# Kernel tuning notes

Hardware: AMD Instinct MI355X
Metric: run time of the kernel (lower is better)

Reference implementation:

```python
import jax, jax.numpy as jnp
import numpy as np
import math

D_MODEL = 1024
NHEAD = 16
D_K = D_MODEL // NHEAD
B, S = 4, 2048


def _stable_softmax(scores):
    # faithful to the source: max-subtract, exp, divide by (sum + 1e-10)
    m = jnp.max(scores, axis=-1, keepdims=True)
    e = jnp.exp(scores - m)
    return e / (jnp.sum(e, axis=-1, keepdims=True) + 1e-10)


def setup_inputs() -> dict:
    key = jax.random.key(0)
    ks = jax.random.split(key, 11)
    gain = math.sqrt(2.0)
    # xavier_uniform: bound = gain * sqrt(6/(fan_in+fan_out)) = gain*sqrt(6/(2*d))
    bound = gain * math.sqrt(6.0 / (2 * D_MODEL))
    def xavier(k):
        return jax.random.uniform(k, (D_MODEL, D_MODEL), jnp.float32, -bound, bound)
    return {
        "q": jax.random.normal(ks[0], (B, S, D_MODEL), jnp.float32),
        "k": jax.random.normal(ks[1], (B, S, D_MODEL), jnp.float32),
        "v": jax.random.normal(ks[2], (B, S, D_MODEL), jnp.float32),
        "Wq": xavier(ks[3]), "bq": jnp.zeros((D_MODEL,), jnp.float32),
        "Wk": xavier(ks[4]), "bk": jnp.zeros((D_MODEL,), jnp.float32),
        "Wv": xavier(ks[5]), "bv": jnp.zeros((D_MODEL,), jnp.float32),
        "Wo": xavier(ks[6]), "bo": jnp.zeros((D_MODEL,), jnp.float32),
    }


def reference(q, k, v, Wq, bq, Wk, bk, Wv, bv, Wo, bo):
    b = q.shape[0]
    # linear projections (torch Linear: x @ W.T + b)
    Q = q @ Wq.T + bq
    K = k @ Wk.T + bk
    V = v @ Wv.T + bv
    # [B, H, S, d_k]
    Q = Q.reshape(b, -1, NHEAD, D_K).transpose(0, 2, 1, 3)
    K = K.reshape(b, -1, NHEAD, D_K).transpose(0, 2, 1, 3)
    V = V.reshape(b, -1, NHEAD, D_K).transpose(0, 2, 1, 3)
    scores = jnp.einsum("bhqd,bhkd->bhqk", Q / math.sqrt(D_K), K)
    attn_weight = _stable_softmax(scores)  # dropout p=0 -> identity
    attn = jnp.einsum("bhqk,bhkd->bhqd", attn_weight, V)
    concat = attn.transpose(0, 2, 1, 3).reshape(b, -1, D_MODEL)
    return concat @ Wo.T + bo
```

## Files before the change

kernel.cpp:

```cpp
#include <hip/hip_runtime.h>

#define DMODEL 1024
#define NH 16
#define DK 64
#define NB 4
#define SEQ 2048
#define MTOT (NB*SEQ)

typedef __attribute__((ext_vector_type(8))) short bf16x8;
typedef __attribute__((ext_vector_type(4))) short s16x4;
typedef __attribute__((ext_vector_type(4))) float f32x4;
typedef __attribute__((ext_vector_type(4))) float f4;
typedef __attribute__((ext_vector_type(4))) unsigned short us4;
typedef __attribute__((ext_vector_type(8))) unsigned short us8;
typedef __attribute__((ext_vector_type(2))) unsigned int u32x2;
typedef const __attribute__((address_space(1))) void* as1cv;
typedef __attribute__((address_space(3))) void* as3v;

__device__ __forceinline__ unsigned short f2bf(float f){
  union { float f; unsigned u; } v; v.f = f;
  unsigned r = v.u + 0x7FFFu + ((v.u >> 16) & 1u);
  return (unsigned short)(r >> 16);
}

__device__ __forceinline__ unsigned cvt_pk_bf16(float lo, float hi){
  unsigned r;
  asm("v_cvt_pk_bf16_f32 %0, %1, %2" : "=v"(r) : "v"(lo), "v"(hi));
  return r;
}

__device__ __forceinline__ f32x4 mfma16(s16x4 a, s16x4 b, f32x4 c){
#if __has_builtin(__builtin_amdgcn_mfma_f32_16x16x16bf16_1k)
  return __builtin_amdgcn_mfma_f32_16x16x16bf16_1k(a, b, c, 0, 0, 0);
#else
  asm("v_mfma_f32_16x16x16_bf16 %0, %1, %2, %0" : "+v"(c) : "v"(a), "v"(b));
  return c;
#endif
}

__global__ __launch_bounds__(256) void cvt_kernel(const float* __restrict__ src,
                                                  unsigned short* __restrict__ dst, int n4){
  int i = blockIdx.x*256 + threadIdx.x;
  if (i >= n4) return;
  f4 f = ((const f4*)src)[i];
  us4 o;
  o.x = f2bf(f.x); o.y = f2bf(f.y); o.z = f2bf(f.z); o.w = f2bf(f.w);
  ((us4*)dst)[i] = o;
}

template<int MODE, int AF32>
__global__ __launch_bounds__(256) void gemm_bt(const void* __restrict__ Aptr,
    const unsigned short* __restrict__ Bw, const float* __restrict__ bias,
    void* __restrict__ dst, float scale)
{
  __shared__ __align__(16) unsigned short sA[128*32];
  __shared__ __align__(16) unsigned short sB[128*32];
  const int tid = threadIdx.x;
  const int lane = tid & 63;
  const int w = tid >> 6;
  const int m0 = blockIdx.y * 128;
  const int n0 = blockIdx.x * 128;
  const int fr = lane & 15;
  const int kg = lane >> 4;
  const int msub = (w & 1) * 64;
  const int nsub = (w >> 1) * 64;

  f32x4 acc[4][4];
#pragma unroll
  for (int i = 0; i < 4; i++)
#pragma unroll
    for (int j = 0; j < 4; j++) acc[i][j] = f32x4{0.f,0.f,0.f,0.f};

  for (int kt = 0; kt < DMODEL; kt += 32){
#pragma unroll
    for (int j = 0; j < 2; j++){
      const int idx = j*256 + tid;
      const int row = idx >> 2;
      const int cg  = (idx & 3) << 3;
      if (AF32){
        const float* ap = (const float*)Aptr + (size_t)(m0+row)*DMODEL + kt + cg;
        f4 f0 = *(const f4*)ap;
        f4 f1 = *(const f4*)(ap + 4);
        us8 o;
        o[0]=f2bf(f0.x); o[1]=f2bf(f0.y); o[2]=f2bf(f0.z); o[3]=f2bf(f0.w);
        o[4]=f2bf(f1.x); o[5]=f2bf(f1.y); o[6]=f2bf(f1.z); o[7]=f2bf(f1.w);
        *((us8*)sA + idx) = o;
      } else {
        const unsigned short* ap = (const unsigned short*)Aptr + (size_t)(m0+row)*DMODEL + kt + cg;
        __builtin_amdgcn_global_load_lds((as1cv)ap, (as3v)(&sA[(size_t)idx*8]), 16, 0, 0);
      }
      const unsigned short* bp = Bw + (size_t)(n0+row)*DMODEL + kt + cg;
      __builtin_amdgcn_global_load_lds((as1cv)bp, (as3v)(&sB[(size_t)idx*8]), 16, 0, 0);
    }
    __syncthreads();
    bf16x8 af[4], bfr[4];
#pragma unroll
    for (int f = 0; f < 4; f++)
      af[f] = *(const bf16x8*)&sA[(msub + f*16 + fr)*32 + kg*8];
#pragma unroll
    for (int f = 0; f < 4; f++)
      bfr[f] = *(const bf16x8*)&sB[(nsub + f*16 + fr)*32 + kg*8];
#pragma unroll
    for (int i = 0; i < 4; i++)
#pragma unroll
      for (int j = 0; j < 4; j++)
        acc[i][j] = __builtin_amdgcn_mfma_f32_16x16x32_bf16(af[i], bfr[j], acc[i][j], 0, 0, 0);
    __syncthreads();
  }

#pragma unroll
  for (int i = 0; i < 4; i++){
#pragma unroll
    for (int j = 0; j < 4; j++){
      const int n = n0 + nsub + j*16 + fr;
      const float bv = bias[n];
      if (MODE == 1){
        const int m = m0 + msub + i*16 + kg*4;
        const int b = m >> 11, s = m & (SEQ-1);
        const int h = n >> 6,  d = n & (DK-1);
        us4 pk;
#pragma unroll
        for (int r = 0; r < 4; r++) pk[r] = f2bf(acc[i][j][r] + bv);
        *(us4*)&((unsigned short*)dst)[((size_t)(b*NH+h)*DK + d)*SEQ + s] = pk;
      } else {
#pragma unroll
        for (int r = 0; r < 4; r++){
          const int m = m0 + msub + i*16 + kg*4 + r;
          float vacc = acc[i][j][r] + bv;
          if (MODE == 2){
            ((float*)dst)[(size_t)m*DMODEL + n] = vacc;
          } else {
            const int b = m >> 11, s = m & (SEQ-1);
            const int h = n >> 6,  d = n & (DK-1);
            ((unsigned short*)dst)[((size_t)(b*NH + h)*SEQ + s)*DK + d] = f2bf(vacc * scale);
          }
        }
      }
    }
  }
}

__global__ __launch_bounds__(256) void attn_kernel(const unsigned short* __restrict__ Qh,
    const unsigned short* __restrict__ Kh, const unsigned short* __restrict__ VTh,
    unsigned short* __restrict__ attnO)
{
  const int tid = threadIdx.x;
  const int lane = tid & 63;
  const int w = tid >> 6;
  const int fr = lane & 15;
  const int kg = lane >> 4;
  const int bid = blockIdx.x;
  const int swz = (bid & 7) * 128 + (bid >> 3);
  const int bh = swz >> 4;
  const int qt = (swz & 15) * 128 + w * 32;

  const unsigned short* Qb = Qh + ((size_t)bh*SEQ + qt)*DK;
  const unsigned short* Kb = Kh + (size_t)bh*SEQ*DK + (size_t)fr*DK + kg*8;
  const unsigned short* Vb = VTh + (size_t)bh*DK*SEQ + kg*4;

  bf16x8 qf[2][2];
#pragma unroll
  for (int qh = 0; qh < 2; qh++){
    qf[qh][0] = *(const bf16x8*)(Qb + (qh*16 + fr)*DK + kg*8);
    qf[qh][1] = *(const bf16x8*)(Qb + (qh*16 + fr)*DK + 32 + kg*8);
  }

  f32x4 o[2][4];
#pragma unroll
  for (int qh = 0; qh < 2; qh++)
#pragma unroll
    for (int nd = 0; nd < 4; nd++) o[qh][nd] = f32x4{0.f,0.f,0.f,0.f};
  float mr[2] = {-1e30f, -1e30f};
  float lr[2] = {0.f, 0.f};

  for (int kt = 0; kt < SEQ; kt += 64){
    f32x4 s[2][4];
#pragma unroll
    for (int n = 0; n < 4; n++){
      const unsigned short* kp = Kb + (size_t)(kt + n*16)*DK;
      bf16x8 k0 = *(const bf16x8*)kp;
      bf16x8 k1 = *(const bf16x8*)(kp + 32);
#pragma unroll
      for (int qh = 0; qh < 2; qh++){
        f32x4 z = f32x4{0.f,0.f,0.f,0.f};
        z         = __builtin_amdgcn_mfma_f32_16x16x32_bf16(k0, qf[qh][0], z, 0, 0, 0);
        s[qh][n]  = __builtin_amdgcn_mfma_f32_16x16x32_bf16(k1, qf[qh][1], s[qh][n] = z, 0, 0, 0);
      }
    }

    unsigned pk[2][4][2];
#pragma unroll
    for (int qh = 0; qh < 2; qh++){
      float tm = -1e30f;
#pragma unroll
      for (int n = 0; n < 4; n++)
#pragma unroll
        for (int r = 0; r < 4; r++) tm = fmaxf(tm, s[qh][n][r]);
      tm = fmaxf(tm, __shfl_xor(tm, 16));
      tm = fmaxf(tm, __shfl_xor(tm, 32));
      const bool defer = __all(tm - mr[qh] <= 8.0f);
      float aal = 1.0f;
      if (!defer){
        const float mn = fmaxf(mr[qh], tm);
        aal = exp2f(mr[qh] - mn);
        mr[qh] = mn;
      }
      float p[4][4];
      float rs = 0.f;
#pragma unroll
      for (int n = 0; n < 4; n++)
#pragma unroll
        for (int r = 0; r < 4; r++){
          p[n][r] = exp2f(s[qh][n][r] - mr[qh]);
          rs += p[n][r];
        }
      rs += __shfl_xor(rs, 16);
      rs += __shfl_xor(rs, 32);
      lr[qh] = lr[qh]*aal + rs;
      if (!defer){
        f32x4 alv;
#pragma unroll
        for (int r = 0; r < 4; r++) alv[r] = __shfl(aal, kg*4 + r, 64);
#pragma unroll
        for (int nd = 0; nd < 4; nd++) o[qh][nd] *= alv;
      }
#pragma unroll
      for (int n = 0; n < 4; n++){
        pk[qh][n][0] = cvt_pk_bf16(p[n][0], p[n][1]);
        pk[qh][n][1] = cvt_pk_bf16(p[n][2], p[n][3]);
      }
    }

#pragma unroll
    for (int nd = 0; nd < 4; nd++){
      const unsigned short* vp = Vb + (size_t)(nd*16 + fr)*SEQ + kt;
      s16x4 vf[4];
#pragma unroll
      for (int ks = 0; ks < 4; ks++) vf[ks] = *(const s16x4*)(vp + ks*16);
#pragma unroll
      for (int ks = 0; ks < 4; ks++){
#pragma unroll
        for (int qh = 0; qh < 2; qh++){
          union { u32x2 u; s16x4 s; } pa;
          pa.u = u32x2{pk[qh][ks][0], pk[qh][ks][1]};
          o[qh][nd] = mfma16(pa.s, vf[ks], o[qh][nd]);
        }
      }
    }
  }

  const int b = bh >> 4, h = bh & (NH-1);
#pragma unroll
  for (int qh = 0; qh < 2; qh++){
    const float invl = 1.f / (lr[qh] + 1e-10f);
    f32x4 iv;
#pragma unroll
    for (int r = 0; r < 4; r++) iv[r] = __shfl(invl, kg*4 + r, 64);
#pragma unroll
    for (int r = 0; r < 4; r++){
      const int srow = qt + qh*16 + kg*4 + r;
      const size_t base = ((size_t)b*SEQ + srow)*DMODEL + (size_t)h*DK;
#pragma unroll
      for (int nd = 0; nd < 4; nd++)
        attnO[base + nd*16 + fr] = f2bf(o[qh][nd][r] * iv[r]);
    }
  }
}

extern "C" void kernel_launch(void* const* d_in, const int* in_sizes, int n_in,
                              void* d_out, int out_size, void* d_ws, size_t ws_size,
                              hipStream_t stream)
{
  const float* q  = (const float*)d_in[0];
  const float* k  = (const float*)d_in[1];
  const float* v  = (const float*)d_in[2];
  const float* Wq = (const float*)d_in[3];
  const float* bq = (const float*)d_in[4];
  const float* Wk = (const float*)d_in[5];
  const float* bk = (const float*)d_in[6];
  const float* Wv = (const float*)d_in[7];
  const float* bv = (const float*)d_in[8];
  const float* Wo = (const float*)d_in[9];
  const float* bo = (const float*)d_in[10];

  char* ws = (char*)d_ws;
  const size_t WSZ = (size_t)DMODEL*DMODEL*2;
  const size_t SZ  = (size_t)MTOT*DMODEL*2;
  unsigned short* wqb   = (unsigned short*)(ws);
  unsigned short* wkb   = (unsigned short*)(ws + WSZ);
  unsigned short* wvb   = (unsigned short*)(ws + 2*WSZ);
  unsigned short* wob   = (unsigned short*)(ws + 3*WSZ);
  unsigned short* Qh    = (unsigned short*)(ws + 4*WSZ);
  unsigned short* Kh    = (unsigned short*)(ws + 4*WSZ + SZ);
  unsigned short* VTh   = (unsigned short*)(ws + 4*WSZ + 2*SZ);
  unsigned short* attnB = (unsigned short*)(ws + 4*WSZ + 3*SZ);

  const int n4 = DMODEL*DMODEL/4;
  cvt_kernel<<<n4/256, 256, 0, stream>>>(Wq, wqb, n4);
  cvt_kernel<<<n4/256, 256, 0, stream>>>(Wk, wkb, n4);
  cvt_kernel<<<n4/256, 256, 0, stream>>>(Wv, wvb, n4);
  cvt_kernel<<<n4/256, 256, 0, stream>>>(Wo, wob, n4);

  dim3 gproj(DMODEL/128, MTOT/128);
  gemm_bt<0,1><<<gproj, 256, 0, stream>>>(q, wqb, bq, Qh, 0.125f*1.44269504088896f);
  gemm_bt<0,1><<<gproj, 256, 0, stream>>>(k, wkb, bk, Kh, 1.0f);
  gemm_bt<1,1><<<gproj, 256, 0, stream>>>(v, wvb, bv, VTh, 1.0f);

  attn_kernel<<<1024, 256, 0, stream>>>(Qh, Kh, VTh, attnB);

  gemm_bt<2,0><<<gproj, 256, 0, stream>>>(attnB, wob, bo, d_out, 1.0f);
}
```

Measured before the change: 539.0 us.

## Software-pipeline K loads and interleave per-half softmax with MFMA in attention

Prefetches the next K tile into registers while the current tile is processed, and issues all V loads for the tile at the start of each iteration. The two 16-row query halves are now handled in sequence, so the second half's QK MFMAs can overlap the first half's softmax. Launch bounds now request 3 blocks per SM. The extra register-resident K/V buffers raise register pressure, and the occupancy target may cause spills.

```diff
diff --git a/kernel.cpp b/kernel.cpp
--- a/kernel.cpp
+++ b/kernel.cpp
@@ -140,7 +140,7 @@
   }
 }
 
-__global__ __launch_bounds__(256) void attn_kernel(const unsigned short* __restrict__ Qh,
+__global__ __launch_bounds__(256, 3) void attn_kernel(const unsigned short* __restrict__ Qh,
     const unsigned short* __restrict__ Kh, const unsigned short* __restrict__ VTh,
     unsigned short* __restrict__ attnO)
 {
@@ -173,80 +173,141 @@
   float mr[2] = {-1e30f, -1e30f};
   float lr[2] = {0.f, 0.f};
 
+  bf16x8 kc[8];
+#pragma unroll
+  for (int n = 0; n < 4; n++){
+    kc[n*2+0] = *(const bf16x8*)(Kb + (size_t)(n*16)*DK);
+    kc[n*2+1] = *(const bf16x8*)(Kb + (size_t)(n*16)*DK + 32);
+  }
+
   for (int kt = 0; kt < SEQ; kt += 64){
-    f32x4 s[2][4];
+    s16x4 vf[4][4];
+#pragma unroll
+    for (int nd = 0; nd < 4; nd++){
+      const unsigned short* vp = Vb + (size_t)(nd*16 + fr)*SEQ + kt;
+#pragma unroll
+      for (int ks = 0; ks < 4; ks++) vf[nd][ks] = *(const s16x4*)(vp + ks*16);
+    }
+
+    unsigned pk0[4][2], pk1[4][2];
+
+    f32x4 s0[4];
 #pragma unroll
     for (int n = 0; n < 4; n++){
-      const unsigned short* kp = Kb + (size_t)(kt + n*16)*DK;
-      bf16x8 k0 = *(const bf16x8*)kp;
-      bf16x8 k1 = *(const bf16x8*)(kp + 32);
-#pragma unroll
-      for (int qh = 0; qh < 2; qh++){
-        f32x4 z = f32x4{0.f,0.f,0.f,0.f};
-        z         = __builtin_amdgcn_mfma_f32_16x16x32_bf16(k0, qf[qh][0], z, 0, 0, 0);
-        s[qh][n]  = __builtin_amdgcn_mfma_f32_16x16x32_bf16(k1, qf[qh][1], s[qh][n] = z, 0, 0, 0);
-      }
-    }
-
-    unsigned pk[2][4][2];
-#pragma unroll
-    for (int qh = 0; qh < 2; qh++){
+      f32x4 z = f32x4{0.f,0.f,0.f,0.f};
+      z     = __builtin_amdgcn_mfma_f32_16x16x32_bf16(kc[n*2+0], qf[0][0], z, 0, 0, 0);
+      s0[n] = __builtin_amdgcn_mfma_f32_16x16x32_bf16(kc[n*2+1], qf[0][1], z, 0, 0, 0);
+    }
+    {
       float tm = -1e30f;
 #pragma unroll
       for (int n = 0; n < 4; n++)
 #pragma unroll
-        for (int r = 0; r < 4; r++) tm = fmaxf(tm, s[qh][n][r]);
+        for (int r = 0; r < 4; r++) tm = fmaxf(tm, s0[n][r]);
       tm = fmaxf(tm, __shfl_xor(tm, 16));
       tm = fmaxf(tm, __shfl_xor(tm, 32));
-      const bool defer = __all(tm - mr[qh] <= 8.0f);
+      const bool defer = __all(tm - mr[0] <= 8.0f);
       float aal = 1.0f;
       if (!defer){
-        const float mn = fmaxf(mr[qh], tm);
-        aal = exp2f(mr[qh] - mn);
-        mr[qh] = mn;
-      }
-      float p[4][4];
+        const float mn = fmaxf(mr[0], tm);
+        aal = exp2f(mr[0] - mn);
+        mr[0] = mn;
+      }
       float rs = 0.f;
 #pragma unroll
       for (int n = 0; n < 4; n++)
 #pragma unroll
         for (int r = 0; r < 4; r++){
-          p[n][r] = exp2f(s[qh][n][r] - mr[qh]);
-          rs += p[n][r];
+          s0[n][r] = exp2f(s0[n][r] - mr[0]);
+          rs += s0[n][r];
         }
       rs += __shfl_xor(rs, 16);
       rs += __shfl_xor(rs, 32);
-      lr[qh] = lr[qh]*aal + rs;
+      lr[0] = lr[0]*aal + rs;
       if (!defer){
         f32x4 alv;
 #pragma unroll
         for (int r = 0; r < 4; r++) alv[r] = __shfl(aal, kg*4 + r, 64);
 #pragma unroll
-        for (int nd = 0; nd < 4; nd++) o[qh][nd] *= alv;
+        for (int nd = 0; nd < 4; nd++) o[0][nd] *= alv;
       }
 #pragma unroll
       for (int n = 0; n < 4; n++){
-        pk[qh][n][0] = cvt_pk_bf16(p[n][0], p[n][1]);
-        pk[qh][n][1] = cvt_pk_bf16(p[n][2], p[n][3]);
+        pk0[n][0] = cvt_pk_bf16(s0[n][0], s0[n][1]);
+        pk0[n][1] = cvt_pk_bf16(s0[n][2], s0[n][3]);
+      }
+    }
+
+    f32x4 s1[4];
+#pragma unroll
+    for (int n = 0; n < 4; n++){
+      f32x4 z = f32x4{0.f,0.f,0.f,0.f};
+      z     = __builtin_amdgcn_mfma_f32_16x16x32_bf16(kc[n*2+0], qf[1][0], z, 0, 0, 0);
+      s1[n] = __builtin_amdgcn_mfma_f32_16x16x32_bf16(kc[n*2+1], qf[1][1], z, 0, 0, 0);
+    }
+
+    const int ktn = (kt + 64 < SEQ) ? (kt + 64) : 0;
+    bf16x8 kn[8];
+#pragma unroll
+    for (int n = 0; n < 4; n++){
+      kn[n*2+0] = *(const bf16x8*)(Kb + (size_t)(ktn + n*16)*DK);
+      kn[n*2+1] = *(const bf16x8*)(Kb + (size_t)(ktn + n*16)*DK + 32);
+    }
+
+    {
+      float tm = -1e30f;
+#pragma unroll
+      for (int n = 0; n < 4; n++)
+#pragma unroll
+        for (int r = 0; r < 4; r++) tm = fmaxf(tm, s1[n][r]);
+      tm = fmaxf(tm, __shfl_xor(tm, 16));
+      tm = fmaxf(tm, __shfl_xor(tm, 32));
+      const bool defer = __all(tm - mr[1] <= 8.0f);
+      float aal = 1.0f;
+      if (!defer){
+        const float mn = fmaxf(mr[1], tm);
+        aal = exp2f(mr[1] - mn);
+        mr[1] = mn;
+      }
+      float rs = 0.f;
+#pragma unroll
+      for (int n = 0; n < 4; n++)
+#pragma unroll
+        for (int r = 0; r < 4; r++){
+          s1[n][r] = exp2f(s1[n][r] - mr[1]);
+          rs += s1[n][r];
+        }
+      rs += __shfl_xor(rs, 16);
+      rs += __shfl_xor(rs, 32);
+      lr[1] = lr[1]*aal + rs;
+      if (!defer){
+        f32x4 alv;
+#pragma unroll
+        for (int r = 0; r < 4; r++) alv[r] = __shfl(aal, kg*4 + r, 64);
+#pragma unroll
+        for (int nd = 0; nd < 4; nd++) o[1][nd] *= alv;
+      }
+#pragma unroll
+      for (int n = 0; n < 4; n++){
+        pk1[n][0] = cvt_pk_bf16(s1[n][0], s1[n][1]);
+        pk1[n][1] = cvt_pk_bf16(s1[n][2], s1[n][3]);
       }
     }
 
 #pragma unroll
     for (int nd = 0; nd < 4; nd++){
-      const unsigned short* vp = Vb + (size_t)(nd*16 + fr)*SEQ + kt;
-      s16x4 vf[4];
-#pragma unroll
-      for (int ks = 0; ks < 4; ks++) vf[ks] = *(const s16x4*)(vp + ks*16);
 #pragma unroll
       for (int ks = 0; ks < 4; ks++){
-#pragma unroll
-        for (int qh = 0; qh < 2; qh++){
-          union { u32x2 u; s16x4 s; } pa;
-          pa.u = u32x2{pk[qh][ks][0], pk[qh][ks][1]};
-          o[qh][nd] = mfma16(pa.s, vf[ks], o[qh][nd]);
-        }
-      }
-    }
+        union { u32x2 u; s16x4 s; } a0, a1;
+        a0.u = u32x2{pk0[ks][0], pk0[ks][1]};
+        a1.u = u32x2{pk1[ks][0], pk1[ks][1]};
+        o[0][nd] = mfma16(a0.s, vf[nd][ks], o[0][nd]);
+        o[1][nd] = mfma16(a1.s, vf[nd][ks], o[1][nd]);
+      }
+    }
+
+#pragma unroll
+    for (int i = 0; i < 8; i++) kc[i] = kn[i];
   }
 
   const int b = bh >> 4, h = bh & (NH-1);
```

After: 510.3 us. 5.3% less time.
